# Kernel optimization log

Hardware: AMD Instinct MI355X
Metric: run time of the kernel (lower is better)

## Reference

```python
import jax, jax.numpy as jnp
import numpy as np

EPS = 1e-8

def l2norm(x, axis=-1, eps=EPS):
    n = jnp.sqrt(jnp.sum(x * x, axis=axis, keepdims=True)) + eps
    return x / n

def setup_inputs() -> dict:
    key = jax.random.key(0)
    k1, k2, k3, k4 = jax.random.split(key, 4)
    B, Q, S, D, SIM = 512, 64, 36, 1024, 256
    query = jax.random.normal(k1, (B, Q, D), dtype=jnp.float32)
    context = jax.random.normal(k2, (B, S, D), dtype=jnp.float32)
    matrix = jax.random.uniform(k3, (B, Q, D), dtype=jnp.float32)
    W = jax.random.normal(k4, (SIM, D), dtype=jnp.float32) * 0.02
    b = jnp.zeros((SIM,), dtype=jnp.float32)
    return {"query": query, "context": context, "matrix": matrix,
            "W": W, "b": b, "smooth": 9}

def reference(query, context, matrix, W, b, smooth):
    # cross_attention
    q = query * matrix                                  # (B,Q,D)
    attn = jnp.einsum('bsd,bqd->bsq', context, q)       # (B,S,Q)
    attn = jnp.where(attn > 0, attn, 0.1 * attn)        # LeakyReLU(0.1)
    attn = l2norm(attn, axis=-1)                        # l2norm over Q
    attn = jnp.swapaxes(attn, 1, 2)                     # (B,Q,S)
    attn = jax.nn.softmax(attn * smooth, axis=2)        # temperature softmax over S
    wcontext = jnp.einsum('bqs,bsd->bqd', attn, context)
    wcontext = l2norm(wcontext, axis=-1)
    # Alignment_vector: squared diff -> linear -> l2norm
    sim_rep = (query - wcontext) ** 2                   # (B,Q,D)
    sim_rep = jnp.einsum('bqd,kd->bqk', sim_rep, W) + b # (B,Q,SIM)
    return l2norm(sim_rep, axis=-1)
```

## Files before the change

### kernel.cpp

```cpp
#include <hip/hip_runtime.h>
#include <hip/hip_bf16.h>

#define BB 512
#define QQ 64
#define SS 36
#define DD 1024
#define SIM 256

typedef unsigned short u16x8 __attribute__((ext_vector_type(8)));
typedef unsigned short u16x4 __attribute__((ext_vector_type(4)));
typedef __bf16 bf16x8 __attribute__((ext_vector_type(8)));
typedef float f32x4 __attribute__((ext_vector_type(4)));
typedef unsigned short us;

__device__ __forceinline__ us f2bf(float f) {
  unsigned u = __float_as_uint(f);
  u += 0x7FFFu + ((u >> 16) & 1u);
  return (us)(u >> 16);
}
__device__ __forceinline__ float bf2f(us h) {
  return __uint_as_float(((unsigned)h) << 16);
}

__global__ __launch_bounds__(256) void k0_w16(const float* __restrict__ W,
                                              us* __restrict__ W16) {
  int i = blockIdx.x * 256 + threadIdx.x;
  float4 v = ((const float4*)W)[i];
  ushort4 p;
  p.x = f2bf(v.x); p.y = f2bf(v.y); p.z = f2bf(v.z); p.w = f2bf(v.w);
  ((ushort4*)W16)[i] = p;
}

__global__ __launch_bounds__(256) void k1_attn(
    const float* __restrict__ query, const float* __restrict__ context,
    const float* __restrict__ matrix, const int* __restrict__ smoothp,
    us* __restrict__ attnBF, us* __restrict__ Gws) {
  __shared__ __align__(16) char smem1[30464];
  us* qmL = (us*)smem1;
  us* ctxL = (us*)(smem1 + 17408);
  float* sc = (float*)smem1;

  const int t = threadIdx.x;
  const int bb = blockIdx.x;
  const int lane = t & 63, w = t >> 6;
  const int ml = lane & 15, kg = lane >> 4;
  const float smf = (float)smoothp[0];

  f32x4 acc[3];
#pragma unroll
  for (int mt = 0; mt < 3; ++mt) acc[mt] = (f32x4){0.f, 0.f, 0.f, 0.f};
  f32x4 accg[3];
#pragma unroll
  for (int j = 0; j < 3; ++j) accg[j] = (f32x4){0.f, 0.f, 0.f, 0.f};

  for (int ch = 0; ch < 8; ++ch) {
    const int d0 = ch * 128;
#pragma unroll
    for (int i = 0; i < 4; ++i) {
      int idx = t + 256 * i;
      int row = idx >> 4, c8 = idx & 15;
      const float4* gq = (const float4*)&query[((size_t)bb * QQ + row) * DD + d0 + c8 * 8];
      const float4* gm = (const float4*)&matrix[((size_t)bb * QQ + row) * DD + d0 + c8 * 8];
      float4 a0 = gq[0], a1 = gq[1], m0 = gm[0], m1 = gm[1];
      u16x8 pk;
      pk[0] = f2bf(a0.x * m0.x); pk[1] = f2bf(a0.y * m0.y);
      pk[2] = f2bf(a0.z * m0.z); pk[3] = f2bf(a0.w * m0.w);
      pk[4] = f2bf(a1.x * m1.x); pk[5] = f2bf(a1.y * m1.y);
      pk[6] = f2bf(a1.z * m1.z); pk[7] = f2bf(a1.w * m1.w);
      *(u16x8*)&qmL[row * 136 + c8 * 8] = pk;
    }
#pragma unroll
    for (int i = 0; i < 3; ++i) {
      int idx = t + 256 * i;
      int row = idx >> 4, c8 = idx & 15;
      u16x8 pk = (u16x8){0, 0, 0, 0, 0, 0, 0, 0};
      if (row < 36) {
        const float4* gc = (const float4*)&context[((size_t)bb * SS + row) * DD + d0 + c8 * 8];
        float4 a0 = gc[0], a1 = gc[1];
        pk[0] = f2bf(a0.x); pk[1] = f2bf(a0.y); pk[2] = f2bf(a0.z); pk[3] = f2bf(a0.w);
        pk[4] = f2bf(a1.x); pk[5] = f2bf(a1.y); pk[6] = f2bf(a1.z); pk[7] = f2bf(a1.w);
      }
      *(u16x8*)&ctxL[row * 136 + c8 * 8] = pk;
    }
    __syncthreads();
#pragma unroll
    for (int ks = 0; ks < 4; ++ks) {
      const int ko = ks * 32 + kg * 8;
      bf16x8 bfrag = __builtin_bit_cast(bf16x8, *(const u16x8*)&qmL[(w * 16 + ml) * 136 + ko]);
      bf16x8 af0 = __builtin_bit_cast(bf16x8, *(const u16x8*)&ctxL[(0 + ml) * 136 + ko]);
      bf16x8 af1 = __builtin_bit_cast(bf16x8, *(const u16x8*)&ctxL[(16 + ml) * 136 + ko]);
      bf16x8 af2 = __builtin_bit_cast(bf16x8, *(const u16x8*)&ctxL[(32 + ml) * 136 + ko]);
      acc[0] = __builtin_amdgcn_mfma_f32_16x16x32_bf16(af0, bfrag, acc[0], 0, 0, 0);
      acc[1] = __builtin_amdgcn_mfma_f32_16x16x32_bf16(af1, bfrag, acc[1], 0, 0, 0);
      acc[2] = __builtin_amdgcn_mfma_f32_16x16x32_bf16(af2, bfrag, acc[2], 0, 0, 0);
      if (w < 3) {
        bf16x8 ai = __builtin_bit_cast(bf16x8, *(const u16x8*)&ctxL[(w * 16 + ml) * 136 + ko]);
        accg[0] = __builtin_amdgcn_mfma_f32_16x16x32_bf16(ai, af0, accg[0], 0, 0, 0);
        accg[1] = __builtin_amdgcn_mfma_f32_16x16x32_bf16(ai, af1, accg[1], 0, 0, 0);
        accg[2] = __builtin_amdgcn_mfma_f32_16x16x32_bf16(ai, af2, accg[2], 0, 0, 0);
      }
    }
    __syncthreads();
  }

  if (w < 3) {
#pragma unroll
    for (int j = 0; j < 3; ++j)
#pragma unroll
      for (int ii = 0; ii < 4; ++ii)
        Gws[(size_t)bb * 2304 + (w * 16 + kg * 4 + ii) * 48 + j * 16 + ml] = f2bf(accg[j][ii]);
  }
#pragma unroll
  for (int mt = 0; mt < 3; ++mt)
#pragma unroll
    for (int ii = 0; ii < 4; ++ii) {
      float v = acc[mt][ii];
      v = v > 0.f ? v : 0.1f * v;
      sc[(mt * 16 + kg * 4 + ii) * 68 + w * 16 + ml] = v;
    }
  __syncthreads();

  if (t < 36) {
    float ssum = 0.f;
    for (int qi = 0; qi < 64; ++qi) { float v = sc[t * 68 + qi]; ssum = fmaf(v, v, ssum); }
    float rn = 1.f / (sqrtf(ssum) + 1e-8f);
    for (int qi = 0; qi < 64; ++qi) sc[t * 68 + qi] *= rn;
  }
  __syncthreads();

  if (t < 64) {
    float mx = -1e30f;
    for (int s2 = 0; s2 < 36; ++s2) mx = fmaxf(mx, sc[s2 * 68 + t]);
    float sum = 0.f;
    float ev[36];
    for (int s2 = 0; s2 < 36; ++s2) {
      float e = __expf((sc[s2 * 68 + t] - mx) * smf);
      ev[s2] = e;
      sum += e;
    }
    float rs = 1.f / sum;
    size_t base = (size_t)bb * (QQ * SS) + t * SS;
#pragma unroll
    for (int s2 = 0; s2 < 36; ++s2) attnBF[base + s2] = f2bf(ev[s2] * rs);
  }
}

template <bool USE_W16>
__global__ __launch_bounds__(512, 4) void k2_fused(
    const float* __restrict__ query, const float* __restrict__ context,
    const float* __restrict__ Wm, const float* __restrict__ bvec,
    const us* __restrict__ attnBF, const us* __restrict__ Gws,
    const us* __restrict__ W16, float* __restrict__ out) {
  __shared__ __align__(16) char smem[49664];
  us* P16s = (us*)smem;
  us* ctxTs = (us*)(smem + 9216);
  us* A16s = (us*)(smem + 28672);
  us* Gf16L = (us*)(smem + 28672);
  float* biasL = (float*)(smem + 46080);
  float* rnL = (float*)(smem + 47104);
  float* rsum = (float*)(smem + 47360);

  const int t = threadIdx.x, bb = blockIdx.x;
  const int lane = t & 63, w = t >> 6;
  const int ml = lane & 15, kg = lane >> 4;

  for (int idx = t; idx < 2304; idx += 512) ((unsigned*)P16s)[idx] = 0;
  for (int idx = t; idx < 1728; idx += 512) ((unsigned*)Gf16L)[idx] = 0;
  for (int idx = t; idx < 1792; idx += 512) {
    int r = idx / 14, c = idx - r * 14;
    *(unsigned*)&ctxTs[r * 76 + 36 + c * 2] = 0;
  }
  if (t < 256) biasL[t] = bvec[t];
  __syncthreads();
  for (int idx = t; idx < 1152; idx += 512) {
    int q = idx / 18, c2 = idx - q * 18;
    *(unsigned*)&P16s[q * 72 + c2 * 2] = ((const unsigned*)attnBF)[(size_t)bb * 1152 + idx];
  }
  for (int idx = t; idx < 1152; idx += 512) {
    int r = idx / 24, c2 = idx - r * 24;
    *(unsigned*)&Gf16L[r * 72 + c2 * 2] = ((const unsigned*)Gws)[(size_t)bb * 1152 + idx];
  }
  __syncthreads();

  if (w < 3) {
    f32x4 accv[4];
#pragma unroll
    for (int mt = 0; mt < 4; ++mt) accv[mt] = (f32x4){0.f, 0.f, 0.f, 0.f};
#pragma unroll
    for (int ks = 0; ks < 2; ++ks) {
      const int ko = ks * 32 + kg * 8;
      bf16x8 gfr = __builtin_bit_cast(bf16x8, *(const u16x8*)&Gf16L[(w * 16 + ml) * 72 + ko]);
#pragma unroll
      for (int mt = 0; mt < 4; ++mt) {
        bf16x8 pf = __builtin_bit_cast(bf16x8, *(const u16x8*)&P16s[(mt * 16 + ml) * 72 + ko]);
        accv[mt] = __builtin_amdgcn_mfma_f32_16x16x32_bf16(pf, gfr, accv[mt], 0, 0, 0);
      }
    }
#pragma unroll
    for (int mt = 0; mt < 4; ++mt)
#pragma unroll
      for (int ii = 0; ii < 4; ++ii) {
        int q = mt * 16 + kg * 4 + ii;
        float vv = accv[mt][ii] * bf2f(P16s[q * 72 + w * 16 + ml]);
        vv += __shfl_xor(vv, 1);
        vv += __shfl_xor(vv, 2);
        vv += __shfl_xor(vv, 4);
        vv += __shfl_xor(vv, 8);
        if (ml == 0) rsum[q * 4 + w] = vv;
      }
  }
  __syncthreads();
  if (t < 64) {
    float s2 = rsum[t * 4] + rsum[t * 4 + 1] + rsum[t * 4 + 2];
    rnL[t] = 1.f / (sqrtf(s2) + 1e-8f);
  }

  f32x4 accs[4][2];
#pragma unroll
  for (int mt = 0; mt < 4; ++mt)
#pragma unroll
    for (int ntl = 0; ntl < 2; ++ntl) accs[mt][ntl] = (f32x4){0.f, 0.f, 0.f, 0.f};

  for (int ch = 0; ch < 8; ++ch) {
    const int d0 = ch * 128;
    for (int idx = t; idx < 1152; idx += 512) {
      int d = idx & 127, s0 = (idx >> 7) * 4;
      const float* cp = &context[((size_t)bb * SS + s0) * DD + d0 + d];
      u16x4 pk;
      pk[0] = f2bf(cp[0]);
      pk[1] = f2bf(cp[DD]);
      pk[2] = f2bf(cp[2 * DD]);
      pk[3] = f2bf(cp[3 * DD]);
      *(u16x4*)&ctxTs[d * 76 + s0] = pk;
    }
    __syncthreads();
    f32x4 aw[4];
#pragma unroll
    for (int mt = 0; mt < 4; ++mt) aw[mt] = (f32x4){0.f, 0.f, 0.f, 0.f};
#pragma unroll
    for (int ks = 0; ks < 2; ++ks) {
      const int ko = ks * 32 + kg * 8;
      u16x4 blo = *(const u16x4*)&ctxTs[(w * 16 + ml) * 76 + ko];
      u16x4 bhi = *(const u16x4*)&ctxTs[(w * 16 + ml) * 76 + ko + 4];
      bf16x8 bfr = __builtin_bit_cast(bf16x8, __builtin_shufflevector(blo, bhi, 0, 1, 2, 3, 4, 5, 6, 7));
#pragma unroll
      for (int mt = 0; mt < 4; ++mt) {
        bf16x8 af = __builtin_bit_cast(bf16x8, *(const u16x8*)&P16s[(mt * 16 + ml) * 72 + ko]);
        aw[mt] = __builtin_amdgcn_mfma_f32_16x16x32_bf16(af, bfr, aw[mt], 0, 0, 0);
      }
    }
#pragma unroll
    for (int mt = 0; mt < 4; ++mt)
#pragma unroll
      for (int ii = 0; ii < 4; ++ii) {
        int q = mt * 16 + kg * 4 + ii;
        float qv = query[((size_t)bb * QQ + q) * DD + d0 + w * 16 + ml];
        float av = qv - aw[mt][ii] * rnL[q];
        A16s[q * 136 + w * 16 + ml] = f2bf(av * av);
      }
    __syncthreads();
#pragma unroll
    for (int ks = 0; ks < 4; ++ks) {
      const int ko = ks * 32 + kg * 8;
      bf16x8 bfr[2];
#pragma unroll
      for (int ntl = 0; ntl < 2; ++ntl) {
        const size_t wrow = (size_t)(w * 32 + ntl * 16 + ml);
        if constexpr (USE_W16) {
          bfr[ntl] = __builtin_bit_cast(bf16x8, *(const u16x8*)&W16[wrow * DD + d0 + ko]);
        } else {
          const float4* wp = (const float4*)&Wm[wrow * DD + d0 + ko];
          float4 x = wp[0], y = wp[1];
          u16x8 pk;
          pk[0] = f2bf(x.x); pk[1] = f2bf(x.y); pk[2] = f2bf(x.z); pk[3] = f2bf(x.w);
          pk[4] = f2bf(y.x); pk[5] = f2bf(y.y); pk[6] = f2bf(y.z); pk[7] = f2bf(y.w);
          bfr[ntl] = __builtin_bit_cast(bf16x8, pk);
        }
      }
#pragma unroll
      for (int mt = 0; mt < 4; ++mt) {
        bf16x8 af = __builtin_bit_cast(bf16x8, *(const u16x8*)&A16s[(mt * 16 + ml) * 136 + ko]);
#pragma unroll
        for (int ntl = 0; ntl < 2; ++ntl)
          accs[mt][ntl] = __builtin_amdgcn_mfma_f32_16x16x32_bf16(af, bfr[ntl], accs[mt][ntl], 0, 0, 0);
      }
    }
    __syncthreads();
  }

#pragma unroll
  for (int mt = 0; mt < 4; ++mt)
#pragma unroll
    for (int ii = 0; ii < 4; ++ii) {
      int q = mt * 16 + kg * 4 + ii;
      float partial = 0.f;
#pragma unroll
      for (int ntl = 0; ntl < 2; ++ntl) {
        int col = w * 32 + ntl * 16 + ml;
        float v = accs[mt][ntl][ii] + biasL[col];
        partial = fmaf(v, v, partial);
      }
      partial += __shfl_xor(partial, 1);
      partial += __shfl_xor(partial, 2);
      partial += __shfl_xor(partial, 4);
      partial += __shfl_xor(partial, 8);
      if (ml == 0) rsum[q * 9 + w] = partial;
    }
  __syncthreads();
  if (t < 64) {
    float ssum = 0.f;
#pragma unroll
    for (int w2 = 0; w2 < 8; ++w2) ssum += rsum[t * 9 + w2];
    rnL[t] = 1.f / (sqrtf(ssum) + 1e-8f);
  }
  __syncthreads();
#pragma unroll
  for (int mt = 0; mt < 4; ++mt)
#pragma unroll
    for (int ntl = 0; ntl < 2; ++ntl)
#pragma unroll
      for (int ii = 0; ii < 4; ++ii) {
        int q = mt * 16 + kg * 4 + ii;
        int col = w * 32 + ntl * 16 + ml;
        float v = accs[mt][ntl][ii] + biasL[col];
        out[((size_t)bb * QQ + q) * SIM + col] = v * rnL[q];
      }
}

extern "C" void kernel_launch(void* const* d_in, const int* in_sizes, int n_in,
                              void* d_out, int out_size, void* d_ws, size_t ws_size,
                              hipStream_t stream) {
  const float* query = (const float*)d_in[0];
  const float* context = (const float*)d_in[1];
  const float* matrix = (const float*)d_in[2];
  const float* Wm = (const float*)d_in[3];
  const float* bvec = (const float*)d_in[4];
  const int* smoothp = (const int*)d_in[5];
  float* out = (float*)d_out;

  const size_t attnB = (size_t)BB * QQ * SS * 2;
  us* attnBF = (us*)d_ws;
  us* Gws = (us*)((char*)d_ws + attnB);
  us* W16 = (us*)((char*)d_ws + 2 * attnB);
  const bool useW16 = ws_size >= 2 * attnB + (size_t)SIM * DD * 2;

  k1_attn<<<dim3(BB), dim3(256), 0, stream>>>(query, context, matrix, smoothp, attnBF, Gws);
  if (useW16) {
    k0_w16<<<dim3(SIM * DD / 1024), dim3(256), 0, stream>>>(Wm, W16);
    k2_fused<true><<<dim3(BB), dim3(512), 0, stream>>>(query, context, Wm, bvec, attnBF, Gws, W16, out);
  } else {
    k2_fused<false><<<dim3(BB), dim3(512), 0, stream>>>(query, context, Wm, bvec, attnBF, Gws, W16, out);
  }
}
```

Before: 169.1 us.

## Split context Gram computation into separate blocks in attention kernel

Launches twice as many k1 blocks. The extra blocks compute only the context Gram matrix (ctx·ctxᵀ) for one batch, and the original blocks compute only the attention scores and softmax. This takes the Gram MFMAs off the critical path of the attention blocks and adds parallelism. The cost is that each context tile is now read and converted from global memory twice. It also packs the attention bf16 stores into pairs.

After: 162.1 us. -4.2%, faster.

```diff
diff --git a/kernel.cpp b/kernel.cpp
--- a/kernel.cpp
+++ b/kernel.cpp
@@ -36,22 +36,67 @@
     const float* __restrict__ matrix, const int* __restrict__ smoothp,
     us* __restrict__ attnBF, us* __restrict__ Gws) {
   __shared__ __align__(16) char smem1[30464];
+
+  const int t = threadIdx.x;
+  const int lane = t & 63, w = t >> 6;
+  const int ml = lane & 15, kg = lane >> 4;
+
+  if (blockIdx.x >= BB) {
+    const int bb = blockIdx.x - BB;
+    us* ctxL = (us*)smem1;
+    f32x4 accg[3];
+#pragma unroll
+    for (int j = 0; j < 3; ++j) accg[j] = (f32x4){0.f, 0.f, 0.f, 0.f};
+
+    for (int ch = 0; ch < 8; ++ch) {
+      const int d0 = ch * 128;
+#pragma unroll
+      for (int i = 0; i < 3; ++i) {
+        int idx = t + 256 * i;
+        int row = idx >> 4, c8 = idx & 15;
+        u16x8 pk = (u16x8){0, 0, 0, 0, 0, 0, 0, 0};
+        if (row < 36) {
+          const float4* gc = (const float4*)&context[((size_t)bb * SS + row) * DD + d0 + c8 * 8];
+          float4 a0 = gc[0], a1 = gc[1];
+          pk[0] = f2bf(a0.x); pk[1] = f2bf(a0.y); pk[2] = f2bf(a0.z); pk[3] = f2bf(a0.w);
+          pk[4] = f2bf(a1.x); pk[5] = f2bf(a1.y); pk[6] = f2bf(a1.z); pk[7] = f2bf(a1.w);
+        }
+        *(u16x8*)&ctxL[row * 136 + c8 * 8] = pk;
+      }
+      __syncthreads();
+      if (w < 3) {
+#pragma unroll
+        for (int ks = 0; ks < 4; ++ks) {
+          const int ko = ks * 32 + kg * 8;
+          bf16x8 ai = __builtin_bit_cast(bf16x8, *(const u16x8*)&ctxL[(w * 16 + ml) * 136 + ko]);
+#pragma unroll
+          for (int j = 0; j < 3; ++j) {
+            bf16x8 af = __builtin_bit_cast(bf16x8, *(const u16x8*)&ctxL[(j * 16 + ml) * 136 + ko]);
+            accg[j] = __builtin_amdgcn_mfma_f32_16x16x32_bf16(ai, af, accg[j], 0, 0, 0);
+          }
+        }
+      }
+      __syncthreads();
+    }
+    if (w < 3) {
+#pragma unroll
+      for (int j = 0; j < 3; ++j)
+#pragma unroll
+        for (int ii = 0; ii < 4; ++ii)
+          Gws[(size_t)bb * 2304 + (w * 16 + kg * 4 + ii) * 48 + j * 16 + ml] = f2bf(accg[j][ii]);
+    }
+    return;
+  }
+
+  const int bb = blockIdx.x;
   us* qmL = (us*)smem1;
   us* ctxL = (us*)(smem1 + 17408);
   float* sc = (float*)smem1;
-
-  const int t = threadIdx.x;
-  const int bb = blockIdx.x;
-  const int lane = t & 63, w = t >> 6;
-  const int ml = lane & 15, kg = lane >> 4;
   const float smf = (float)smoothp[0];
 
   f32x4 acc[3];
 #pragma unroll
   for (int mt = 0; mt < 3; ++mt) acc[mt] = (f32x4){0.f, 0.f, 0.f, 0.f};
-  f32x4 accg[3];
-#pragma unroll
-  for (int j = 0; j < 3; ++j) accg[j] = (f32x4){0.f, 0.f, 0.f, 0.f};
 
   for (int ch = 0; ch < 8; ++ch) {
     const int d0 = ch * 128;
@@ -87,29 +132,16 @@
     for (int ks = 0; ks < 4; ++ks) {
       const int ko = ks * 32 + kg * 8;
       bf16x8 bfrag = __builtin_bit_cast(bf16x8, *(const u16x8*)&qmL[(w * 16 + ml) * 136 + ko]);
-      bf16x8 af0 = __builtin_bit_cast(bf16x8, *(const u16x8*)&ctxL[(0 + ml) * 136 + ko]);
-      bf16x8 af1 = __builtin_bit_cast(bf16x8, *(const u16x8*)&ctxL[(16 + ml) * 136 + ko]);
-      bf16x8 af2 = __builtin_bit_cast(bf16x8, *(const u16x8*)&ctxL[(32 + ml) * 136 + ko]);
-      acc[0] = __builtin_amdgcn_mfma_f32_16x16x32_bf16(af0, bfrag, acc[0], 0, 0, 0);
-      acc[1] = __builtin_amdgcn_mfma_f32_16x16x32_bf16(af1, bfrag, acc[1], 0, 0, 0);
-      acc[2] = __builtin_amdgcn_mfma_f32_16x16x32_bf16(af2, bfrag, acc[2], 0, 0, 0);
-      if (w < 3) {
-        bf16x8 ai = __builtin_bit_cast(bf16x8, *(const u16x8*)&ctxL[(w * 16 + ml) * 136 + ko]);
-        accg[0] = __builtin_amdgcn_mfma_f32_16x16x32_bf16(ai, af0, accg[0], 0, 0, 0);
-        accg[1] = __builtin_amdgcn_mfma_f32_16x16x32_bf16(ai, af1, accg[1], 0, 0, 0);
-        accg[2] = __builtin_amdgcn_mfma_f32_16x16x32_bf16(ai, af2, accg[2], 0, 0, 0);
-      }
-    }
-    __syncthreads();
-  }
-
-  if (w < 3) {
-#pragma unroll
-    for (int j = 0; j < 3; ++j)
-#pragma unroll
-      for (int ii = 0; ii < 4; ++ii)
-        Gws[(size_t)bb * 2304 + (w * 16 + kg * 4 + ii) * 48 + j * 16 + ml] = f2bf(accg[j][ii]);
-  }
+#pragma unroll
+      for (int mt = 0; mt < 3; ++mt) {
+        bf16x8 afrag =
+            __builtin_bit_cast(bf16x8, *(const u16x8*)&ctxL[(mt * 16 + ml) * 136 + ko]);
+        acc[mt] = __builtin_amdgcn_mfma_f32_16x16x32_bf16(afrag, bfrag, acc[mt], 0, 0, 0);
+      }
+    }
+    __syncthreads();
+  }
+
 #pragma unroll
   for (int mt = 0; mt < 3; ++mt)
 #pragma unroll
@@ -141,7 +173,12 @@
     float rs = 1.f / sum;
     size_t base = (size_t)bb * (QQ * SS) + t * SS;
 #pragma unroll
-    for (int s2 = 0; s2 < 36; ++s2) attnBF[base + s2] = f2bf(ev[s2] * rs);
+    for (int s2 = 0; s2 < 36; s2 += 2) {
+      ushort2 p;
+      p.x = f2bf(ev[s2] * rs);
+      p.y = f2bf(ev[s2 + 1] * rs);
+      *(ushort2*)&attnBF[base + s2] = p;
+    }
   }
 }
 
@@ -344,7 +381,7 @@
   us* W16 = (us*)((char*)d_ws + 2 * attnB);
   const bool useW16 = ws_size >= 2 * attnB + (size_t)SIM * DD * 2;
 
-  k1_attn<<<dim3(BB), dim3(256), 0, stream>>>(query, context, matrix, smoothp, attnBF, Gws);
+  k1_attn<<<dim3(2 * BB), dim3(256), 0, stream>>>(query, context, matrix, smoothp, attnBF, Gws);
   if (useW16) {
     k0_w16<<<dim3(SIM * DD / 1024), dim3(256), 0, stream>>>(Wm, W16);
     k2_fused<true><<<dim3(BB), dim3(512), 0, stream>>>(query, context, Wm, bvec, attnBF, Gws, W16, out);
```

## Double the k1 block to 512 threads and prefetch next chunk into registers

Applied to the files above, without the earlier changes.

The attention kernel now launches 512 threads per batch. Its MFMA work is split across 8 waves, so each wave handles either two context tiles or one tile plus the Gram-matrix tiles. The global loads for the next 128-wide D chunk are issued into registers before the MFMA loop, overlapping memory latency with compute. The softmax output is also written as paired ushort2 stores. The register prefetch raises VGPR pressure under the stricter launch bound, and the Gram work stays unevenly distributed across waves.

Result: slower. 174.1 us (+3.0%).

```diff
diff --git a/kernel.cpp b/kernel.cpp
--- a/kernel.cpp
+++ b/kernel.cpp
@@ -31,7 +31,7 @@
   ((ushort4*)W16)[i] = p;
 }
 
-__global__ __launch_bounds__(256) void k1_attn(
+__global__ __launch_bounds__(512, 4) void k1_attn(
     const float* __restrict__ query, const float* __restrict__ context,
     const float* __restrict__ matrix, const int* __restrict__ smoothp,
     us* __restrict__ attnBF, us* __restrict__ Gws) {
@@ -44,80 +44,118 @@
   const int bb = blockIdx.x;
   const int lane = t & 63, w = t >> 6;
   const int ml = lane & 15, kg = lane >> 4;
+  const int nt = w >> 1;
   const float smf = (float)smoothp[0];
 
-  f32x4 acc[3];
-#pragma unroll
-  for (int mt = 0; mt < 3; ++mt) acc[mt] = (f32x4){0.f, 0.f, 0.f, 0.f};
-  f32x4 accg[3];
-#pragma unroll
-  for (int j = 0; j < 3; ++j) accg[j] = (f32x4){0.f, 0.f, 0.f, 0.f};
-
+  const int qr0 = t >> 4, qc0 = (t & 15) * 8;
+  const int qr1 = (t + 512) >> 4, qc1 = qc0;
+  const int cr0 = t >> 4;
+  const int cr1 = (t + 512) >> 4;
+
+  float4 pq0a, pq0b, pm0a, pm0b, pq1a, pq1b, pm1a, pm1b;
+  float4 pc0a, pc0b, pc1a, pc1b;
+
+#define K1_LOAD(d0)                                                            \
+  {                                                                            \
+    const float4* gq0 = (const float4*)&query[((size_t)bb * QQ + qr0) * DD + (d0) + qc0]; \
+    const float4* gm0 = (const float4*)&matrix[((size_t)bb * QQ + qr0) * DD + (d0) + qc0]; \
+    pq0a = gq0[0]; pq0b = gq0[1]; pm0a = gm0[0]; pm0b = gm0[1];                \
+    const float4* gq1 = (const float4*)&query[((size_t)bb * QQ + qr1) * DD + (d0) + qc1]; \
+    const float4* gm1 = (const float4*)&matrix[((size_t)bb * QQ + qr1) * DD + (d0) + qc1]; \
+    pq1a = gq1[0]; pq1b = gq1[1]; pm1a = gm1[0]; pm1b = gm1[1];                \
+    pc0a = pc0b = pc1a = pc1b = (float4){0.f, 0.f, 0.f, 0.f};                  \
+    if (cr0 < 36) {                                                            \
+      const float4* gc = (const float4*)&context[((size_t)bb * SS + cr0) * DD + (d0) + qc0]; \
+      pc0a = gc[0]; pc0b = gc[1];                                              \
+    }                                                                          \
+    if (t < 256 && cr1 < 36) {                                                 \
+      const float4* gc = (const float4*)&context[((size_t)bb * SS + cr1) * DD + (d0) + qc1]; \
+      pc1a = gc[0]; pc1b = gc[1];                                              \
+    }                                                                          \
+  }
+
+  f32x4 acc0 = (f32x4){0.f, 0.f, 0.f, 0.f};
+  f32x4 acc1 = (f32x4){0.f, 0.f, 0.f, 0.f};
+  f32x4 gacc[3];
+#pragma unroll
+  for (int j = 0; j < 3; ++j) gacc[j] = (f32x4){0.f, 0.f, 0.f, 0.f};
+
+  K1_LOAD(0);
   for (int ch = 0; ch < 8; ++ch) {
-    const int d0 = ch * 128;
-#pragma unroll
-    for (int i = 0; i < 4; ++i) {
-      int idx = t + 256 * i;
-      int row = idx >> 4, c8 = idx & 15;
-      const float4* gq = (const float4*)&query[((size_t)bb * QQ + row) * DD + d0 + c8 * 8];
-      const float4* gm = (const float4*)&matrix[((size_t)bb * QQ + row) * DD + d0 + c8 * 8];
-      float4 a0 = gq[0], a1 = gq[1], m0 = gm[0], m1 = gm[1];
+    __syncthreads();
+    {
       u16x8 pk;
-      pk[0] = f2bf(a0.x * m0.x); pk[1] = f2bf(a0.y * m0.y);
-      pk[2] = f2bf(a0.z * m0.z); pk[3] = f2bf(a0.w * m0.w);
-      pk[4] = f2bf(a1.x * m1.x); pk[5] = f2bf(a1.y * m1.y);
-      pk[6] = f2bf(a1.z * m1.z); pk[7] = f2bf(a1.w * m1.w);
-      *(u16x8*)&qmL[row * 136 + c8 * 8] = pk;
-    }
-#pragma unroll
-    for (int i = 0; i < 3; ++i) {
-      int idx = t + 256 * i;
-      int row = idx >> 4, c8 = idx & 15;
-      u16x8 pk = (u16x8){0, 0, 0, 0, 0, 0, 0, 0};
-      if (row < 36) {
-        const float4* gc = (const float4*)&context[((size_t)bb * SS + row) * DD + d0 + c8 * 8];
-        float4 a0 = gc[0], a1 = gc[1];
-        pk[0] = f2bf(a0.x); pk[1] = f2bf(a0.y); pk[2] = f2bf(a0.z); pk[3] = f2bf(a0.w);
-        pk[4] = f2bf(a1.x); pk[5] = f2bf(a1.y); pk[6] = f2bf(a1.z); pk[7] = f2bf(a1.w);
-      }
-      *(u16x8*)&ctxL[row * 136 + c8 * 8] = pk;
-    }
+      pk[0] = f2bf(pq0a.x * pm0a.x); pk[1] = f2bf(pq0a.y * pm0a.y);
+      pk[2] = f2bf(pq0a.z * pm0a.z); pk[3] = f2bf(pq0a.w * pm0a.w);
+      pk[4] = f2bf(pq0b.x * pm0b.x); pk[5] = f2bf(pq0b.y * pm0b.y);
+      pk[6] = f2bf(pq0b.z * pm0b.z); pk[7] = f2bf(pq0b.w * pm0b.w);
+      *(u16x8*)&qmL[qr0 * 136 + qc0] = pk;
+      pk[0] = f2bf(pq1a.x * pm1a.x); pk[1] = f2bf(pq1a.y * pm1a.y);
+      pk[2] = f2bf(pq1a.z * pm1a.z); pk[3] = f2bf(pq1a.w * pm1a.w);
+      pk[4] = f2bf(pq1b.x * pm1b.x); pk[5] = f2bf(pq1b.y * pm1b.y);
+      pk[6] = f2bf(pq1b.z * pm1b.z); pk[7] = f2bf(pq1b.w * pm1b.w);
+      *(u16x8*)&qmL[qr1 * 136 + qc1] = pk;
+      pk[0] = f2bf(pc0a.x); pk[1] = f2bf(pc0a.y); pk[2] = f2bf(pc0a.z); pk[3] = f2bf(pc0a.w);
+      pk[4] = f2bf(pc0b.x); pk[5] = f2bf(pc0b.y); pk[6] = f2bf(pc0b.z); pk[7] = f2bf(pc0b.w);
+      *(u16x8*)&ctxL[cr0 * 136 + qc0] = pk;
+      if (t < 256) {
+        pk[0] = f2bf(pc1a.x); pk[1] = f2bf(pc1a.y); pk[2] = f2bf(pc1a.z); pk[3] = f2bf(pc1a.w);
+        pk[4] = f2bf(pc1b.x); pk[5] = f2bf(pc1b.y); pk[6] = f2bf(pc1b.z); pk[7] = f2bf(pc1b.w);
+        *(u16x8*)&ctxL[cr1 * 136 + qc1] = pk;
+      }
+    }
+    if (ch < 7) K1_LOAD((ch + 1) * 128);
     __syncthreads();
 #pragma unroll
     for (int ks = 0; ks < 4; ++ks) {
       const int ko = ks * 32 + kg * 8;
-      bf16x8 bfrag = __builtin_bit_cast(bf16x8, *(const u16x8*)&qmL[(w * 16 + ml) * 136 + ko]);
-      bf16x8 af0 = __builtin_bit_cast(bf16x8, *(const u16x8*)&ctxL[(0 + ml) * 136 + ko]);
-      bf16x8 af1 = __builtin_bit_cast(bf16x8, *(const u16x8*)&ctxL[(16 + ml) * 136 + ko]);
-      bf16x8 af2 = __builtin_bit_cast(bf16x8, *(const u16x8*)&ctxL[(32 + ml) * 136 + ko]);
-      acc[0] = __builtin_amdgcn_mfma_f32_16x16x32_bf16(af0, bfrag, acc[0], 0, 0, 0);
-      acc[1] = __builtin_amdgcn_mfma_f32_16x16x32_bf16(af1, bfrag, acc[1], 0, 0, 0);
-      acc[2] = __builtin_amdgcn_mfma_f32_16x16x32_bf16(af2, bfrag, acc[2], 0, 0, 0);
-      if (w < 3) {
-        bf16x8 ai = __builtin_bit_cast(bf16x8, *(const u16x8*)&ctxL[(w * 16 + ml) * 136 + ko]);
-        accg[0] = __builtin_amdgcn_mfma_f32_16x16x32_bf16(ai, af0, accg[0], 0, 0, 0);
-        accg[1] = __builtin_amdgcn_mfma_f32_16x16x32_bf16(ai, af1, accg[1], 0, 0, 0);
-        accg[2] = __builtin_amdgcn_mfma_f32_16x16x32_bf16(ai, af2, accg[2], 0, 0, 0);
-      }
-    }
-    __syncthreads();
-  }
-
-  if (w < 3) {
+      bf16x8 bq = __builtin_bit_cast(bf16x8, *(const u16x8*)&qmL[(nt * 16 + ml) * 136 + ko]);
+      if ((w & 1) == 0) {
+        bf16x8 af0 = __builtin_bit_cast(bf16x8, *(const u16x8*)&ctxL[(0 + ml) * 136 + ko]);
+        bf16x8 af1 = __builtin_bit_cast(bf16x8, *(const u16x8*)&ctxL[(16 + ml) * 136 + ko]);
+        acc0 = __builtin_amdgcn_mfma_f32_16x16x32_bf16(af0, bq, acc0, 0, 0, 0);
+        acc1 = __builtin_amdgcn_mfma_f32_16x16x32_bf16(af1, bq, acc1, 0, 0, 0);
+      } else {
+        bf16x8 af2 = __builtin_bit_cast(bf16x8, *(const u16x8*)&ctxL[(32 + ml) * 136 + ko]);
+        acc0 = __builtin_amdgcn_mfma_f32_16x16x32_bf16(af2, bq, acc0, 0, 0, 0);
+        if (w < 6) {
+          bf16x8 ai = __builtin_bit_cast(bf16x8, *(const u16x8*)&ctxL[(nt * 16 + ml) * 136 + ko]);
+#pragma unroll
+          for (int j = 0; j < 3; ++j) {
+            bf16x8 aj = __builtin_bit_cast(bf16x8, *(const u16x8*)&ctxL[(j * 16 + ml) * 136 + ko]);
+            gacc[j] = __builtin_amdgcn_mfma_f32_16x16x32_bf16(ai, aj, gacc[j], 0, 0, 0);
+          }
+        }
+      }
+    }
+  }
+  __syncthreads();
+
+  if ((w & 1) && w < 6) {
 #pragma unroll
     for (int j = 0; j < 3; ++j)
 #pragma unroll
       for (int ii = 0; ii < 4; ++ii)
-        Gws[(size_t)bb * 2304 + (w * 16 + kg * 4 + ii) * 48 + j * 16 + ml] = f2bf(accg[j][ii]);
-  }
-#pragma unroll
-  for (int mt = 0; mt < 3; ++mt)
+        Gws[(size_t)bb * 2304 + (nt * 16 + kg * 4 + ii) * 48 + j * 16 + ml] = f2bf(gacc[j][ii]);
+  }
+  if ((w & 1) == 0) {
 #pragma unroll
     for (int ii = 0; ii < 4; ++ii) {
-      float v = acc[mt][ii];
+      float v0 = acc0[ii];
+      v0 = v0 > 0.f ? v0 : 0.1f * v0;
+      sc[(0 + kg * 4 + ii) * 68 + nt * 16 + ml] = v0;
+      float v1 = acc1[ii];
+      v1 = v1 > 0.f ? v1 : 0.1f * v1;
+      sc[(16 + kg * 4 + ii) * 68 + nt * 16 + ml] = v1;
+    }
+  } else {
+#pragma unroll
+    for (int ii = 0; ii < 4; ++ii) {
+      float v = acc0[ii];
       v = v > 0.f ? v : 0.1f * v;
-      sc[(mt * 16 + kg * 4 + ii) * 68 + w * 16 + ml] = v;
-    }
+      sc[(32 + kg * 4 + ii) * 68 + nt * 16 + ml] = v;
+    }
+  }
   __syncthreads();
 
   if (t < 36) {
@@ -141,7 +179,12 @@
     float rs = 1.f / sum;
     size_t base = (size_t)bb * (QQ * SS) + t * SS;
 #pragma unroll
-    for (int s2 = 0; s2 < 36; ++s2) attnBF[base + s2] = f2bf(ev[s2] * rs);
+    for (int s2 = 0; s2 < 36; s2 += 2) {
+      ushort2 p;
+      p.x = f2bf(ev[s2] * rs);
+      p.y = f2bf(ev[s2 + 1] * rs);
+      *(ushort2*)&attnBF[base + s2] = p;
+    }
   }
 }
 
@@ -344,7 +387,7 @@
   us* W16 = (us*)((char*)d_ws + 2 * attnB);
   const bool useW16 = ws_size >= 2 * attnB + (size_t)SIM * DD * 2;
 
-  k1_attn<<<dim3(BB), dim3(256), 0, stream>>>(query, context, matrix, smoothp, attnBF, Gws);
+  k1_attn<<<dim3(BB), dim3(512), 0, stream>>>(query, context, matrix, smoothp, attnBF, Gws);
   if (useW16) {
     k0_w16<<<dim3(SIM * DD / 1024), dim3(256), 0, stream>>>(Wm, W16);
     k2_fused<true><<<dim3(BB), dim3(512), 0, stream>>>(query, context, Wm, bvec, attnBF, Gws, W16, out);
```

## Restructure attention kernel to stream query·matrix from registers with larger context tiles

Applied to the files above, without the earlier changes.

k1_attn now stages context in two 512-wide halves in shared memory instead of eight 128-wide chunks. The query*matrix B-fragments are loaded straight from global memory into registers with software prefetch, so they no longer pass through LDS, and the Gram-matrix MFMAs move to a separate loop. The attention output is written as packed pairs, and k2 rotates its d-chunk start per block to spread memory traffic. The larger LDS footprint (about 62KB) may limit occupancy, and the per-lane strided global loads may coalesce less well.

Result: no change. 167.9 us (-0.7%).

```diff
diff --git a/kernel.cpp b/kernel.cpp
--- a/kernel.cpp
+++ b/kernel.cpp
@@ -31,14 +31,13 @@
   ((ushort4*)W16)[i] = p;
 }
 
-__global__ __launch_bounds__(256) void k1_attn(
+__global__ __launch_bounds__(256, 2) void k1_attn(
     const float* __restrict__ query, const float* __restrict__ context,
     const float* __restrict__ matrix, const int* __restrict__ smoothp,
     us* __restrict__ attnBF, us* __restrict__ Gws) {
-  __shared__ __align__(16) char smem1[30464];
-  us* qmL = (us*)smem1;
-  us* ctxL = (us*)(smem1 + 17408);
-  float* sc = (float*)smem1;
+  __shared__ __align__(16) char smem1[62976];
+  us* ctxL = (us*)smem1;
+  float* sc = (float*)(smem1 + 49920);
 
   const int t = threadIdx.x;
   const int bb = blockIdx.x;
@@ -46,58 +45,70 @@
   const int ml = lane & 15, kg = lane >> 4;
   const float smf = (float)smoothp[0];
 
+  for (int idx = t; idx < 3120; idx += 256)
+    ((unsigned*)(ctxL + 36 * 520))[idx] = 0;
+
+  const size_t qmoff = ((size_t)bb * QQ + w * 16 + ml) * DD + kg * 8;
+  const float* qrow = query + qmoff;
+  const float* mrow = matrix + qmoff;
+
   f32x4 acc[3];
 #pragma unroll
   for (int mt = 0; mt < 3; ++mt) acc[mt] = (f32x4){0.f, 0.f, 0.f, 0.f};
-  f32x4 accg[3];
-#pragma unroll
-  for (int j = 0; j < 3; ++j) accg[j] = (f32x4){0.f, 0.f, 0.f, 0.f};
-
-  for (int ch = 0; ch < 8; ++ch) {
-    const int d0 = ch * 128;
-#pragma unroll
-    for (int i = 0; i < 4; ++i) {
+  f32x4 gacc[3];
+#pragma unroll
+  for (int j = 0; j < 3; ++j) gacc[j] = (f32x4){0.f, 0.f, 0.f, 0.f};
+
+  for (int h = 0; h < 2; ++h) {
+    const int db = h * 512;
+#pragma unroll
+    for (int i = 0; i < 18; ++i) {
       int idx = t + 256 * i;
-      int row = idx >> 4, c8 = idx & 15;
-      const float4* gq = (const float4*)&query[((size_t)bb * QQ + row) * DD + d0 + c8 * 8];
-      const float4* gm = (const float4*)&matrix[((size_t)bb * QQ + row) * DD + d0 + c8 * 8];
-      float4 a0 = gq[0], a1 = gq[1], m0 = gm[0], m1 = gm[1];
+      int row = idx >> 7, c4 = (idx & 127) * 4;
+      float4 v = *(const float4*)&context[((size_t)bb * SS + row) * DD + db + c4];
+      ushort4 p;
+      p.x = f2bf(v.x); p.y = f2bf(v.y); p.z = f2bf(v.z); p.w = f2bf(v.w);
+      *(ushort4*)&ctxL[row * 520 + c4] = p;
+    }
+    __syncthreads();
+
+    float4 qa = *(const float4*)(qrow + db);
+    float4 qb = *(const float4*)(qrow + db + 4);
+    float4 ma = *(const float4*)(mrow + db);
+    float4 mb = *(const float4*)(mrow + db + 4);
+#pragma unroll
+    for (int ks = 0; ks < 16; ++ks) {
       u16x8 pk;
-      pk[0] = f2bf(a0.x * m0.x); pk[1] = f2bf(a0.y * m0.y);
-      pk[2] = f2bf(a0.z * m0.z); pk[3] = f2bf(a0.w * m0.w);
-      pk[4] = f2bf(a1.x * m1.x); pk[5] = f2bf(a1.y * m1.y);
-      pk[6] = f2bf(a1.z * m1.z); pk[7] = f2bf(a1.w * m1.w);
-      *(u16x8*)&qmL[row * 136 + c8 * 8] = pk;
-    }
-#pragma unroll
-    for (int i = 0; i < 3; ++i) {
-      int idx = t + 256 * i;
-      int row = idx >> 4, c8 = idx & 15;
-      u16x8 pk = (u16x8){0, 0, 0, 0, 0, 0, 0, 0};
-      if (row < 36) {
-        const float4* gc = (const float4*)&context[((size_t)bb * SS + row) * DD + d0 + c8 * 8];
-        float4 a0 = gc[0], a1 = gc[1];
-        pk[0] = f2bf(a0.x); pk[1] = f2bf(a0.y); pk[2] = f2bf(a0.z); pk[3] = f2bf(a0.w);
-        pk[4] = f2bf(a1.x); pk[5] = f2bf(a1.y); pk[6] = f2bf(a1.z); pk[7] = f2bf(a1.w);
-      }
-      *(u16x8*)&ctxL[row * 136 + c8 * 8] = pk;
-    }
-    __syncthreads();
-#pragma unroll
-    for (int ks = 0; ks < 4; ++ks) {
+      pk[0] = f2bf(qa.x * ma.x); pk[1] = f2bf(qa.y * ma.y);
+      pk[2] = f2bf(qa.z * ma.z); pk[3] = f2bf(qa.w * ma.w);
+      pk[4] = f2bf(qb.x * mb.x); pk[5] = f2bf(qb.y * mb.y);
+      pk[6] = f2bf(qb.z * mb.z); pk[7] = f2bf(qb.w * mb.w);
+      if (ks < 15) {
+        const float* q2 = qrow + db + (ks + 1) * 32;
+        const float* m2 = mrow + db + (ks + 1) * 32;
+        qa = *(const float4*)q2; qb = *(const float4*)(q2 + 4);
+        ma = *(const float4*)m2; mb = *(const float4*)(m2 + 4);
+      }
+      bf16x8 bq = __builtin_bit_cast(bf16x8, pk);
       const int ko = ks * 32 + kg * 8;
-      bf16x8 bfrag = __builtin_bit_cast(bf16x8, *(const u16x8*)&qmL[(w * 16 + ml) * 136 + ko]);
-      bf16x8 af0 = __builtin_bit_cast(bf16x8, *(const u16x8*)&ctxL[(0 + ml) * 136 + ko]);
-      bf16x8 af1 = __builtin_bit_cast(bf16x8, *(const u16x8*)&ctxL[(16 + ml) * 136 + ko]);
-      bf16x8 af2 = __builtin_bit_cast(bf16x8, *(const u16x8*)&ctxL[(32 + ml) * 136 + ko]);
-      acc[0] = __builtin_amdgcn_mfma_f32_16x16x32_bf16(af0, bfrag, acc[0], 0, 0, 0);
-      acc[1] = __builtin_amdgcn_mfma_f32_16x16x32_bf16(af1, bfrag, acc[1], 0, 0, 0);
-      acc[2] = __builtin_amdgcn_mfma_f32_16x16x32_bf16(af2, bfrag, acc[2], 0, 0, 0);
-      if (w < 3) {
-        bf16x8 ai = __builtin_bit_cast(bf16x8, *(const u16x8*)&ctxL[(w * 16 + ml) * 136 + ko]);
-        accg[0] = __builtin_amdgcn_mfma_f32_16x16x32_bf16(ai, af0, accg[0], 0, 0, 0);
-        accg[1] = __builtin_amdgcn_mfma_f32_16x16x32_bf16(ai, af1, accg[1], 0, 0, 0);
-        accg[2] = __builtin_amdgcn_mfma_f32_16x16x32_bf16(ai, af2, accg[2], 0, 0, 0);
+      bf16x8 a0 = __builtin_bit_cast(bf16x8, *(const u16x8*)&ctxL[(0 + ml) * 520 + ko]);
+      bf16x8 a1 = __builtin_bit_cast(bf16x8, *(const u16x8*)&ctxL[(16 + ml) * 520 + ko]);
+      bf16x8 a2 = __builtin_bit_cast(bf16x8, *(const u16x8*)&ctxL[(32 + ml) * 520 + ko]);
+      acc[0] = __builtin_amdgcn_mfma_f32_16x16x32_bf16(a0, bq, acc[0], 0, 0, 0);
+      acc[1] = __builtin_amdgcn_mfma_f32_16x16x32_bf16(a1, bq, acc[1], 0, 0, 0);
+      acc[2] = __builtin_amdgcn_mfma_f32_16x16x32_bf16(a2, bq, acc[2], 0, 0, 0);
+    }
+
+    if (w < 3) {
+#pragma unroll
+      for (int ks = 0; ks < 16; ++ks) {
+        const int ko = ks * 32 + kg * 8;
+        bf16x8 ai = __builtin_bit_cast(bf16x8, *(const u16x8*)&ctxL[(w * 16 + ml) * 520 + ko]);
+#pragma unroll
+        for (int j = 0; j < 3; ++j) {
+          bf16x8 aj = __builtin_bit_cast(bf16x8, *(const u16x8*)&ctxL[(j * 16 + ml) * 520 + ko]);
+          gacc[j] = __builtin_amdgcn_mfma_f32_16x16x32_bf16(ai, aj, gacc[j], 0, 0, 0);
+        }
       }
     }
     __syncthreads();
@@ -108,7 +119,7 @@
     for (int j = 0; j < 3; ++j)
 #pragma unroll
       for (int ii = 0; ii < 4; ++ii)
-        Gws[(size_t)bb * 2304 + (w * 16 + kg * 4 + ii) * 48 + j * 16 + ml] = f2bf(accg[j][ii]);
+        Gws[(size_t)bb * 2304 + (w * 16 + kg * 4 + ii) * 48 + j * 16 + ml] = f2bf(gacc[j][ii]);
   }
 #pragma unroll
   for (int mt = 0; mt < 3; ++mt)
@@ -141,7 +152,12 @@
     float rs = 1.f / sum;
     size_t base = (size_t)bb * (QQ * SS) + t * SS;
 #pragma unroll
-    for (int s2 = 0; s2 < 36; ++s2) attnBF[base + s2] = f2bf(ev[s2] * rs);
+    for (int s2 = 0; s2 < 36; s2 += 2) {
+      ushort2 p;
+      p.x = f2bf(ev[s2] * rs);
+      p.y = f2bf(ev[s2 + 1] * rs);
+      *(ushort2*)&attnBF[base + s2] = p;
+    }
   }
 }
 
@@ -163,6 +179,7 @@
   const int t = threadIdx.x, bb = blockIdx.x;
   const int lane = t & 63, w = t >> 6;
   const int ml = lane & 15, kg = lane >> 4;
+  const int chs = ((bb >> 3) ^ bb) & 7;
 
   for (int idx = t; idx < 2304; idx += 512) ((unsigned*)P16s)[idx] = 0;
   for (int idx = t; idx < 1728; idx += 512) ((unsigned*)Gf16L)[idx] = 0;
@@ -222,7 +239,7 @@
     for (int ntl = 0; ntl < 2; ++ntl) accs[mt][ntl] = (f32x4){0.f, 0.f, 0.f, 0.f};
 
   for (int ch = 0; ch < 8; ++ch) {
-    const int d0 = ch * 128;
+    const int d0 = ((ch + chs) & 7) * 128;
     for (int idx = t; idx < 1152; idx += 512) {
       int d = idx & 127, s0 = (idx >> 7) * 4;
       const float* cp = &context[((size_t)bb * SS + s0) * DD + d0 + d];
```
